# Performance work log

Hardware: AMD Instinct MI355X
Metric: run time of the kernel (lower is better)

The kernel has to match this reference:

```python
import jax, jax.numpy as jnp
import numpy as np

BS = 131072
NX = 4       # num_dim_x (p, theta, v, omega)
NU = 1       # num_dim_control
H = 256      # n_hidden


def segway_dynamics(x):
    # x: [bs, 4] -> f: [bs, 4], g: [bs, 4, 1]
    theta, v, omega = x[:, 1], x[:, 2], x[:, 3]
    c, s = jnp.cos(theta), jnp.sin(theta)
    f2 = (c * (9.8 * s + 11.5 * v) + 68.4 * v - 1.2 * omega ** 2 * s) / (c - 24.7)
    f3 = (-58.8 * v * c - 243.5 * v - s * (208.3 + omega ** 2 * c)) / (c ** 2 - 24.7)
    f = jnp.stack([v, omega, f2, f3], axis=1)
    g2 = (-1.8 * c - 10.9) / (c - 24.7)
    g3 = (9.3 * c + 38.6) / (c ** 2 - 24.7)
    zero = jnp.zeros_like(g2)
    g = jnp.stack([zero, zero, g2, g3], axis=1)[:, :, None]
    return f, g


def setup_inputs() -> dict:
    key = jax.random.key(0)
    ks = jax.random.split(key, 13)
    d = {"x": jax.random.normal(ks[0], (BS, NX), dtype=jnp.float32)}
    shapes = {
        "Vw1": (H, NX), "Vb1": (H,),
        "Vw2": (H, H),  "Vb2": (H,),
        "Vw3": (H // 4, H), "Vb3": (H // 4,),
        "Uw1": (H, NX), "Ub1": (H,),
        "Uw2": (H, H),  "Ub2": (H,),
        "Uw3": (NU, H), "Ub3": (NU,),
    }
    for i, (name, shp) in enumerate(shapes.items()):
        d[name] = jax.random.normal(ks[i + 1], shp, dtype=jnp.float32) * 0.05
    return d


def reference(x, Vw1, Vb1, Vw2, Vb2, Vw3, Vb3, Uw1, Ub1, Uw2, Ub2, Uw3, Ub3):
    # --- Lyapunov value + analytic gradient ---
    a1 = jnp.tanh(x @ Vw1.T + Vb1)          # [bs, H]
    a2 = jnp.tanh(a1 @ Vw2.T + Vb2)         # [bs, H]
    a3 = jnp.tanh(a2 @ Vw3.T + Vb3)         # [bs, H//4]
    V = 0.5 * jnp.sum(a3 * a3, axis=1)      # [bs]
    # diag_embed(1-tanh^2) @ W  ==  (1-tanh^2)[:, :, None] * W  (no dense diag)
    D1 = (1.0 - a1 ** 2)[:, :, None] * Vw1[None]                          # [bs, H, 4]
    D2 = (1.0 - a2 ** 2)[:, :, None] * jnp.einsum('ij,bjk->bik', Vw2, D1)  # [bs, H, 4]
    D3 = (1.0 - a3 ** 2)[:, :, None] * jnp.einsum('ij,bjk->bik', Vw3, D2)  # [bs, H/4, 4]
    grad_V = jnp.einsum('bi,bij->bj', a3, D3)  # [bs, 4]

    # --- learned controls ---
    u1 = jnp.tanh(x @ Uw1.T + Ub1)
    u2 = jnp.tanh(u1 @ Uw2.T + Ub2)
    u = jnp.tanh(u2 @ Uw3.T + Ub3) * 20.0     # [bs, 1]

    # --- Lie derivatives / Vdot ---
    f, g = segway_dynamics(x)
    L_f_V = jnp.sum(grad_V * f, axis=1, keepdims=True)    # [bs, 1]
    L_g_V = jnp.einsum('bi,bic->bc', grad_V, g)           # [bs, 1]
    Vdot = (L_f_V + jnp.sum(L_g_V * u, axis=1, keepdims=True))[:, :, None]  # [bs,1,1]
    return u, V, Vdot
```

## Files before the change

### kernel.cpp

```cpp
#include <hip/hip_runtime.h>
#include <hip/hip_bf16.h>

#define BSZ 131072

typedef __bf16 v8bf __attribute__((ext_vector_type(8)));
typedef float f32x4 __attribute__((ext_vector_type(4)));

constexpr int RPB = 64;
constexpr int NTHREADS = 512;
constexpr int LDA = 264;

constexpr int OFF_B2T = 0;
constexpr int OFF_U2T = 65536;
constexpr int OFF_B2  = 131072;
constexpr int OFF_B3T = 196608;
constexpr int OFF_B3  = 212992;
constexpr int OFF_U3  = 229376;
constexpr int OFF_GV  = 233472;
constexpr int OFF_LV1 = 237568;
constexpr int OFF_LU1 = 245760;
constexpr int WS_ELEMS = 253952;

__device__ __forceinline__ float tanhf_fast(float x){
  float e = __expf(2.0f * x);
  return 1.0f - 2.0f / (e + 1.0f);
}

__device__ __forceinline__ __bf16 f2bf(float f){
  unsigned u = __builtin_bit_cast(unsigned, f);
  u += 0x8000u;
  unsigned short h = (unsigned short)(u >> 16);
  return __builtin_bit_cast(__bf16, h);
}

__global__ void prep_weights(const float* __restrict__ Vw2,
                             const float* __restrict__ Uw2,
                             const float* __restrict__ Vw3,
                             const float* __restrict__ Vw1,
                             const float* __restrict__ Uw1,
                             const float* __restrict__ Uw3,
                             __bf16* __restrict__ ws){
  int e = blockIdx.x * 256 + threadIdx.x;
  if (e >= WS_ELEMS) return;
  int idx, NT, base, mode; const float* W;
  if      (e <  65536){ idx = e;          W = Vw2; mode = 0; NT = 16; base = OFF_B2T; }
  else if (e < 131072){ idx = e - 65536;  W = Uw2; mode = 0; NT = 16; base = OFF_U2T; }
  else if (e < 196608){ idx = e - 131072; W = Vw2; mode = 1; NT = 16; base = OFF_B2;  }
  else if (e < 212992){ idx = e - 196608; W = Vw3; mode = 0; NT = 4;  base = OFF_B3T; }
  else if (e < 229376){ idx = e - 212992; W = Vw3; mode = 1; NT = 16; base = OFF_B3;  }
  else if (e < 233472){ idx = e - 229376; W = Uw3; mode = 2; NT = 1;  base = OFF_U3;  }
  else if (e < 237568){ idx = e - 233472; W = Vw1; mode = 3; NT = 1;  base = OFF_GV;  }
  else if (e < 245760){ idx = e - 237568; W = Vw1; mode = 4; NT = 16; base = OFF_LV1; }
  else                { idx = e - 245760; W = Uw1; mode = 4; NT = 16; base = OFF_LU1; }
  int j = idx & 7, l = (idx >> 3) & 63, f = idx >> 9;
  int nt = f % NT, ks = f / NT;
  int k = ks * 32 + (l >> 4) * 8 + j;
  int n = nt * 16 + (l & 15);
  float v;
  if      (mode == 0) v = W[n * 256 + k];
  else if (mode == 1) v = W[k * 256 + n];
  else if (mode == 2) v = (n == 0) ? W[k] : 0.0f;
  else if (mode == 3) v = (n < 4)  ? W[k * 4 + n] : 0.0f;
  else                v = (k < 4)  ? W[n * 4 + k] : 0.0f;
  ws[base + idx] = f2bf(v);
}

__global__ __launch_bounds__(NTHREADS, 4) void fused_clf(
    const float* __restrict__ x,
    const float* __restrict__ Vb1, const float* __restrict__ Vb2,
    const float* __restrict__ Vb3,
    const float* __restrict__ Ub1, const float* __restrict__ Ub2,
    const float* __restrict__ Ub3,
    const __bf16* __restrict__ ws,
    float* __restrict__ out)
{
  __shared__ __bf16 b1[RPB][LDA];
  __shared__ __bf16 b2[RPB][LDA];
  __shared__ union alignas(16) S3 {
    __bf16 b3[RPB][72];
    float  r4[8][RPB][4];
  } s3;
  __shared__ float  red[RPB][4];
  __shared__ float  utile[RPB];

  const int tid  = threadIdx.x;
  const int lane = tid & 63;
  const int wave = tid >> 6;
  const int quad = lane >> 4;
  const int l16  = lane & 15;
  const int row0 = blockIdx.x * RPB;

  v8bf xa[4];
  #pragma unroll
  for (int m = 0; m < 4; m++){
    v8bf z;
    #pragma unroll
    for (int j = 0; j < 8; j++) z[j] = (__bf16)0.0f;
    if (quad == 0){
      float4 xv = ((const float4*)x)[row0 + m*16 + l16];
      z[0] = f2bf(xv.x); z[1] = f2bf(xv.y); z[2] = f2bf(xv.z); z[3] = f2bf(xv.w);
    }
    xa[m] = z;
  }

  auto layer1m = [&](const __bf16* __restrict__ Bw, const float* __restrict__ bv,
                     __bf16 (*dst)[LDA]){
    const v8bf* B = (const v8bf*)Bw;
    v8bf bf0 = B[(wave*2 + 0)*64 + lane];
    v8bf bf1 = B[(wave*2 + 1)*64 + lane];
    f32x4 acc[4][2];
    #pragma unroll
    for (int m = 0; m < 4; m++){ f32x4 z={0.f,0.f,0.f,0.f}; acc[m][0]=z; acc[m][1]=z; }
    #pragma unroll
    for (int m = 0; m < 4; m++){
      acc[m][0] = __builtin_amdgcn_mfma_f32_16x16x32_bf16(xa[m], bf0, acc[m][0], 0,0,0);
      acc[m][1] = __builtin_amdgcn_mfma_f32_16x16x32_bf16(xa[m], bf1, acc[m][1], 0,0,0);
    }
    #pragma unroll
    for (int m = 0; m < 4; m++){
      int rb = m*16 + quad*4;
      #pragma unroll
      for (int nt = 0; nt < 2; nt++){
        int col = (wave*2 + nt)*16 + l16;
        float bvv = bv[col];
        #pragma unroll
        for (int r = 0; r < 4; r++)
          dst[rb + r][col] = f2bf(tanhf_fast(acc[m][nt][r] + bvv));
      }
    }
  };

  auto gemm256 = [&](const __bf16 (*A)[LDA], const __bf16* __restrict__ Bw,
                     const float* __restrict__ bias, __bf16 (*dst)[LDA], int epi){
    f32x4 acc[4][2];
    #pragma unroll
    for (int m = 0; m < 4; m++){ f32x4 z={0.f,0.f,0.f,0.f}; acc[m][0]=z; acc[m][1]=z; }
    const v8bf* B = (const v8bf*)Bw;
    #pragma unroll
    for (int kk = 0; kk < 8; kk++){
      v8bf a[4];
      #pragma unroll
      for (int m = 0; m < 4; m++)
        a[m] = *(const v8bf*)&A[m*16 + l16][kk*32 + quad*8];
      #pragma unroll
      for (int nt = 0; nt < 2; nt++){
        v8bf bf = B[(kk*16 + wave*2 + nt)*64 + lane];
        #pragma unroll
        for (int m = 0; m < 4; m++)
          acc[m][nt] = __builtin_amdgcn_mfma_f32_16x16x32_bf16(a[m], bf, acc[m][nt], 0,0,0);
      }
    }
    #pragma unroll
    for (int m = 0; m < 4; m++){
      int rb = m*16 + quad*4;
      #pragma unroll
      for (int nt = 0; nt < 2; nt++){
        int col = (wave*2 + nt)*16 + l16;
        float bvv = (epi == 0) ? bias[col] : 0.0f;
        #pragma unroll
        for (int r = 0; r < 4; r++){
          float v = acc[m][nt][r] + bvv;
          if (epi == 0){
            dst[rb + r][col] = f2bf(tanhf_fast(v));
          } else {
            float a1v = (float)dst[rb + r][col];
            dst[rb + r][col] = f2bf(v * (1.0f - a1v*a1v));
          }
        }
      }
    }
  };

  auto mfma_reduce = [&](const __bf16 (*A)[LDA], const __bf16* __restrict__ Bw,
                         int ncols){
    f32x4 acc[4];
    #pragma unroll
    for (int m = 0; m < 4; m++){ f32x4 z={0.f,0.f,0.f,0.f}; acc[m]=z; }
    const v8bf* B = (const v8bf*)Bw;
    v8bf bf = B[wave*64 + lane];
    #pragma unroll
    for (int m = 0; m < 4; m++){
      v8bf a = *(const v8bf*)&A[m*16 + l16][wave*32 + quad*8];
      acc[m] = __builtin_amdgcn_mfma_f32_16x16x32_bf16(a, bf, acc[m], 0,0,0);
    }
    if (l16 < ncols){
      #pragma unroll
      for (int m = 0; m < 4; m++)
        #pragma unroll
        for (int r = 0; r < 4; r++)
          s3.r4[wave][m*16 + quad*4 + r][l16] = acc[m][r];
    }
  };

  layer1m(ws + OFF_LU1, Ub1, b2);
  __syncthreads();
  gemm256(b2, ws + OFF_U2T, Ub2, b1, 0);
  __syncthreads();
  mfma_reduce(b1, ws + OFF_U3, 1);
  __syncthreads();
  if (tid < RPB){
    float z = Ub3[0];
    #pragma unroll
    for (int w = 0; w < 8; w++) z += s3.r4[w][tid][0];
    float u = tanhf_fast(z) * 20.0f;
    utile[tid] = u;
    out[row0 + tid] = u;
  }
  layer1m(ws + OFF_LV1, Vb1, b1);
  __syncthreads();
  gemm256(b1, ws + OFF_B2T, Vb2, b2, 0);
  __syncthreads();

  {
    const int mp = wave >> 2;
    const int nt = wave & 3;
    f32x4 acc[2];
    { f32x4 z={0.f,0.f,0.f,0.f}; acc[0]=z; acc[1]=z; }
    const v8bf* B = (const v8bf*)(ws + OFF_B3T);
    #pragma unroll
    for (int kk = 0; kk < 8; kk++){
      v8bf bf = B[(kk*4 + nt)*64 + lane];
      #pragma unroll
      for (int m2 = 0; m2 < 2; m2++){
        v8bf a = *(const v8bf*)&b2[(mp*2 + m2)*16 + l16][kk*32 + quad*8];
        acc[m2] = __builtin_amdgcn_mfma_f32_16x16x32_bf16(a, bf, acc[m2], 0,0,0);
      }
    }
    int col = nt*16 + l16;
    float bvv = Vb3[col];
    #pragma unroll
    for (int m2 = 0; m2 < 2; m2++){
      #pragma unroll
      for (int r = 0; r < 4; r++){
        int row = (mp*2 + m2)*16 + quad*4 + r;
        float t = tanhf_fast(acc[m2][r] + bvv);
        float sq = t * t;
        sq += __shfl_xor(sq, 1); sq += __shfl_xor(sq, 2);
        sq += __shfl_xor(sq, 4); sq += __shfl_xor(sq, 8);
        s3.b3[row][col] = f2bf(t * (1.0f - t*t));
        if (l16 == 0) red[row][nt] = sq;
      }
    }
  }
  __syncthreads();

  {
    f32x4 acc[4][2];
    #pragma unroll
    for (int m = 0; m < 4; m++){ f32x4 z={0.f,0.f,0.f,0.f}; acc[m][0]=z; acc[m][1]=z; }
    const v8bf* B = (const v8bf*)(ws + OFF_B3);
    #pragma unroll
    for (int kk = 0; kk < 2; kk++){
      v8bf a[4];
      #pragma unroll
      for (int m = 0; m < 4; m++)
        a[m] = *(const v8bf*)&s3.b3[m*16 + l16][kk*32 + quad*8];
      #pragma unroll
      for (int nt = 0; nt < 2; nt++){
        v8bf bf = B[(kk*16 + wave*2 + nt)*64 + lane];
        #pragma unroll
        for (int m = 0; m < 4; m++)
          acc[m][nt] = __builtin_amdgcn_mfma_f32_16x16x32_bf16(a[m], bf, acc[m][nt], 0,0,0);
      }
    }
    #pragma unroll
    for (int m = 0; m < 4; m++){
      int rb = m*16 + quad*4;
      #pragma unroll
      for (int nt = 0; nt < 2; nt++){
        int col = (wave*2 + nt)*16 + l16;
        #pragma unroll
        for (int r = 0; r < 4; r++){
          float a2v = (float)b2[rb + r][col];
          b2[rb + r][col] = f2bf(acc[m][nt][r] * (1.0f - a2v*a2v));
        }
      }
    }
    if (tid < RPB)
      out[BSZ + row0 + tid] = 0.5f * (red[tid][0] + red[tid][1] + red[tid][2] + red[tid][3]);
  }
  __syncthreads();

  gemm256(b2, ws + OFF_B2, nullptr, b1, 1);
  __syncthreads();
  mfma_reduce(b1, ws + OFF_GV, 4);
  __syncthreads();
  if (tid < 256){
    int b = tid >> 2, k2 = tid & 3;
    float s = 0.f;
    #pragma unroll
    for (int w = 0; w < 8; w++) s += s3.r4[w][b][k2];
    red[b][k2] = s;
  }
  __syncthreads();

  if (tid < RPB){
    float4 xv = ((const float4*)x)[row0 + tid];
    float th = xv.y, vv = xv.z, om = xv.w;
    float c = cosf(th), s = sinf(th);
    float dc  = c - 24.7f;
    float dc2 = c*c - 24.7f;
    float f2v = (c*(9.8f*s + 11.5f*vv) + 68.4f*vv - 1.2f*om*om*s) / dc;
    float f3v = (-58.8f*vv*c - 243.5f*vv - s*(208.3f + om*om*c)) / dc2;
    float g2v = (-1.8f*c - 10.9f) / dc;
    float g3v = (9.3f*c + 38.6f) / dc2;
    float Lf = red[tid][0]*vv + red[tid][1]*om + red[tid][2]*f2v + red[tid][3]*f3v;
    float Lg = red[tid][2]*g2v + red[tid][3]*g3v;
    out[2*BSZ + row0 + tid] = Lf + Lg * utile[tid];
  }
}

extern "C" void kernel_launch(void* const* d_in, const int* in_sizes, int n_in,
                              void* d_out, int out_size, void* d_ws, size_t ws_size,
                              hipStream_t stream) {
  const float* x   = (const float*)d_in[0];
  const float* Vw1 = (const float*)d_in[1];
  const float* Vb1 = (const float*)d_in[2];
  const float* Vw2 = (const float*)d_in[3];
  const float* Vb2 = (const float*)d_in[4];
  const float* Vw3 = (const float*)d_in[5];
  const float* Vb3 = (const float*)d_in[6];
  const float* Uw1 = (const float*)d_in[7];
  const float* Ub1 = (const float*)d_in[8];
  const float* Uw2 = (const float*)d_in[9];
  const float* Ub2 = (const float*)d_in[10];
  const float* Uw3 = (const float*)d_in[11];
  const float* Ub3 = (const float*)d_in[12];
  __bf16* ws = (__bf16*)d_ws;
  float* out = (float*)d_out;

  hipLaunchKernelGGL(prep_weights, dim3((WS_ELEMS + 255) / 256), dim3(256), 0, stream,
                     Vw2, Uw2, Vw3, Vw1, Uw1, Uw3, ws);
  hipLaunchKernelGGL(fused_clf, dim3(BSZ / RPB), dim3(NTHREADS), 0, stream,
                     x, Vb1, Vb2, Vb3, Ub1, Ub2, Ub3, ws, out);
}
```

Baseline: 198.4 us.

## Swap MFMA operand roles to weights-as-A, halve rows per block, pack bf16 stores

Reorients every MFMA so weights are the A operand and batch activations the B operand, which makes accumulator registers run along the feature dimension. Epilogues can then write four contiguous bf16 values with one packed store instead of scattered scalar stores. Rows per block drop from 64 to 32 and the occupancy hint rises to 8 blocks per CU, trading weight reuse per block for more resident blocks. The weight-prep kernel now writes eight elements per thread with vector stores.

```diff
diff --git a/kernel.cpp b/kernel.cpp
--- a/kernel.cpp
+++ b/kernel.cpp
@@ -4,21 +4,23 @@
 #define BSZ 131072
 
 typedef __bf16 v8bf __attribute__((ext_vector_type(8)));
+typedef __bf16 v4bf __attribute__((ext_vector_type(4)));
 typedef float f32x4 __attribute__((ext_vector_type(4)));
 
-constexpr int RPB = 64;
+constexpr int RPB = 32;
 constexpr int NTHREADS = 512;
-constexpr int LDA = 264;
-
-constexpr int OFF_B2T = 0;
-constexpr int OFF_U2T = 65536;
-constexpr int OFF_B2  = 131072;
-constexpr int OFF_B3T = 196608;
-constexpr int OFF_B3  = 212992;
+constexpr int LDA  = 264;
+constexpr int LDA3 = 72;
+
+constexpr int OFF_U2  = 0;
+constexpr int OFF_V2  = 65536;
+constexpr int OFF_V2T = 131072;
+constexpr int OFF_V3  = 196608;
+constexpr int OFF_V3T = 212992;
 constexpr int OFF_U3  = 229376;
 constexpr int OFF_GV  = 233472;
-constexpr int OFF_LV1 = 237568;
-constexpr int OFF_LU1 = 245760;
+constexpr int OFF_L1V = 237568;
+constexpr int OFF_L1U = 245760;
 constexpr int WS_ELEMS = 253952;
 
 __device__ __forceinline__ float tanhf_fast(float x){
@@ -31,6 +33,12 @@
   u += 0x8000u;
   unsigned short h = (unsigned short)(u >> 16);
   return __builtin_bit_cast(__bf16, h);
+}
+
+__device__ __forceinline__ unsigned pack2bf(float lo, float hi){
+  unsigned a = __builtin_bit_cast(unsigned, lo) + 0x8000u;
+  unsigned b = __builtin_bit_cast(unsigned, hi) + 0x8000u;
+  return __builtin_amdgcn_perm(b, a, 0x07060302u);
 }
 
 __global__ void prep_weights(const float* __restrict__ Vw2,
@@ -40,32 +48,39 @@
                              const float* __restrict__ Uw1,
                              const float* __restrict__ Uw3,
                              __bf16* __restrict__ ws){
-  int e = blockIdx.x * 256 + threadIdx.x;
-  if (e >= WS_ELEMS) return;
-  int idx, NT, base, mode; const float* W;
-  if      (e <  65536){ idx = e;          W = Vw2; mode = 0; NT = 16; base = OFF_B2T; }
-  else if (e < 131072){ idx = e - 65536;  W = Uw2; mode = 0; NT = 16; base = OFF_U2T; }
-  else if (e < 196608){ idx = e - 131072; W = Vw2; mode = 1; NT = 16; base = OFF_B2;  }
-  else if (e < 212992){ idx = e - 196608; W = Vw3; mode = 0; NT = 4;  base = OFF_B3T; }
-  else if (e < 229376){ idx = e - 212992; W = Vw3; mode = 1; NT = 16; base = OFF_B3;  }
-  else if (e < 233472){ idx = e - 229376; W = Uw3; mode = 2; NT = 1;  base = OFF_U3;  }
-  else if (e < 237568){ idx = e - 233472; W = Vw1; mode = 3; NT = 1;  base = OFF_GV;  }
-  else if (e < 245760){ idx = e - 237568; W = Vw1; mode = 4; NT = 16; base = OFF_LV1; }
-  else                { idx = e - 245760; W = Uw1; mode = 4; NT = 16; base = OFF_LU1; }
-  int j = idx & 7, l = (idx >> 3) & 63, f = idx >> 9;
-  int nt = f % NT, ks = f / NT;
-  int k = ks * 32 + (l >> 4) * 8 + j;
-  int n = nt * 16 + (l & 15);
-  float v;
-  if      (mode == 0) v = W[n * 256 + k];
-  else if (mode == 1) v = W[k * 256 + n];
-  else if (mode == 2) v = (n == 0) ? W[k] : 0.0f;
-  else if (mode == 3) v = (n < 4)  ? W[k * 4 + n] : 0.0f;
-  else                v = (k < 4)  ? W[n * 4 + k] : 0.0f;
-  ws[base + idx] = f2bf(v);
-}
-
-__global__ __launch_bounds__(NTHREADS, 4) void fused_clf(
+  int e8 = blockIdx.x * 256 + threadIdx.x;
+  if (e8 >= WS_ELEMS / 8) return;
+  int idx8 = e8 * 8;
+  int idx, MT, mode; const float* W;
+  if      (idx8 <  65536){ idx = idx8;          W = Uw2; mode = 0; MT = 16; }
+  else if (idx8 < 131072){ idx = idx8 - 65536;  W = Vw2; mode = 0; MT = 16; }
+  else if (idx8 < 196608){ idx = idx8 - 131072; W = Vw2; mode = 1; MT = 16; }
+  else if (idx8 < 212992){ idx = idx8 - 196608; W = Vw3; mode = 0; MT = 4;  }
+  else if (idx8 < 229376){ idx = idx8 - 212992; W = Vw3; mode = 1; MT = 16; }
+  else if (idx8 < 233472){ idx = idx8 - 229376; W = Uw3; mode = 2; MT = 1;  }
+  else if (idx8 < 237568){ idx = idx8 - 233472; W = Vw1; mode = 3; MT = 1;  }
+  else if (idx8 < 245760){ idx = idx8 - 237568; W = Vw1; mode = 4; MT = 16; }
+  else                   { idx = idx8 - 245760; W = Uw1; mode = 4; MT = 16; }
+  int l = (idx >> 3) & 63, f = idx >> 9;
+  int mt = f % MT, ks = f / MT;
+  int m  = mt * 16 + (l & 15);
+  int k0 = ks * 32 + ((l >> 4) << 3);
+  __bf16 tmp[8];
+  #pragma unroll
+  for (int j = 0; j < 8; j++){
+    int k = k0 + j;
+    float v;
+    if      (mode == 0) v = W[m * 256 + k];
+    else if (mode == 1) v = W[k * 256 + m];
+    else if (mode == 2) v = (m == 0) ? W[k] : 0.0f;
+    else if (mode == 3) v = (m < 4)  ? W[k * 4 + m] : 0.0f;
+    else                v = (k < 4)  ? W[m * 4 + k] : 0.0f;
+    tmp[j] = f2bf(v);
+  }
+  *(uint4*)&ws[idx8] = *(const uint4*)tmp;
+}
+
+__global__ __launch_bounds__(NTHREADS, 8) void fused_clf(
     const float* __restrict__ x,
     const float* __restrict__ Vb1, const float* __restrict__ Vb2,
     const float* __restrict__ Vb3,
@@ -74,14 +89,14 @@
     const __bf16* __restrict__ ws,
     float* __restrict__ out)
 {
-  __shared__ __bf16 b1[RPB][LDA];
-  __shared__ __bf16 b2[RPB][LDA];
+  __shared__ alignas(16) __bf16 b1[RPB][LDA];
+  __shared__ alignas(16) __bf16 b2[RPB][LDA];
   __shared__ union alignas(16) S3 {
-    __bf16 b3[RPB][72];
+    __bf16 b3[RPB][LDA3];
     float  r4[8][RPB][4];
   } s3;
-  __shared__ float  red[RPB][4];
-  __shared__ float  utile[RPB];
+  __shared__ float red[RPB][4];
+  __shared__ float utile[RPB];
 
   const int tid  = threadIdx.x;
   const int lane = tid & 63;
@@ -90,113 +105,117 @@
   const int l16  = lane & 15;
   const int row0 = blockIdx.x * RPB;
 
-  v8bf xa[4];
+  v8bf xb[2];
   #pragma unroll
-  for (int m = 0; m < 4; m++){
+  for (int bt = 0; bt < 2; bt++){
     v8bf z;
     #pragma unroll
     for (int j = 0; j < 8; j++) z[j] = (__bf16)0.0f;
     if (quad == 0){
-      float4 xv = ((const float4*)x)[row0 + m*16 + l16];
+      float4 xv = ((const float4*)x)[row0 + bt*16 + l16];
       z[0] = f2bf(xv.x); z[1] = f2bf(xv.y); z[2] = f2bf(xv.z); z[3] = f2bf(xv.w);
     }
-    xa[m] = z;
-  }
-
-  auto layer1m = [&](const __bf16* __restrict__ Bw, const float* __restrict__ bv,
+    xb[bt] = z;
+  }
+
+  auto layer1m = [&](const __bf16* __restrict__ Aw, const float* __restrict__ bv,
                      __bf16 (*dst)[LDA]){
-    const v8bf* B = (const v8bf*)Bw;
-    v8bf bf0 = B[(wave*2 + 0)*64 + lane];
-    v8bf bf1 = B[(wave*2 + 1)*64 + lane];
-    f32x4 acc[4][2];
-    #pragma unroll
-    for (int m = 0; m < 4; m++){ f32x4 z={0.f,0.f,0.f,0.f}; acc[m][0]=z; acc[m][1]=z; }
-    #pragma unroll
-    for (int m = 0; m < 4; m++){
-      acc[m][0] = __builtin_amdgcn_mfma_f32_16x16x32_bf16(xa[m], bf0, acc[m][0], 0,0,0);
-      acc[m][1] = __builtin_amdgcn_mfma_f32_16x16x32_bf16(xa[m], bf1, acc[m][1], 0,0,0);
-    }
-    #pragma unroll
-    for (int m = 0; m < 4; m++){
-      int rb = m*16 + quad*4;
-      #pragma unroll
-      for (int nt = 0; nt < 2; nt++){
-        int col = (wave*2 + nt)*16 + l16;
-        float bvv = bv[col];
+    const v8bf* A = (const v8bf*)Aw;
+    #pragma unroll
+    for (int mi = 0; mi < 2; mi++){
+      v8bf af = A[(wave*2 + mi)*64 + lane];
+      f32x4 acc[2];
+      { f32x4 z = {0.f,0.f,0.f,0.f}; acc[0]=z; acc[1]=z; }
+      #pragma unroll
+      for (int bt = 0; bt < 2; bt++)
+        acc[bt] = __builtin_amdgcn_mfma_f32_16x16x32_bf16(af, xb[bt], acc[bt], 0,0,0);
+      int f0 = (wave*2 + mi)*16 + quad*4;
+      float4 bv4 = *(const float4*)&bv[f0];
+      #pragma unroll
+      for (int bt = 0; bt < 2; bt++){
+        int b = bt*16 + l16;
+        float t0 = tanhf_fast(acc[bt][0] + bv4.x);
+        float t1 = tanhf_fast(acc[bt][1] + bv4.y);
+        float t2 = tanhf_fast(acc[bt][2] + bv4.z);
+        float t3 = tanhf_fast(acc[bt][3] + bv4.w);
+        uint2 p = { pack2bf(t0, t1), pack2bf(t2, t3) };
+        *(uint2*)&dst[b][f0] = p;
+      }
+    }
+  };
+
+  auto gemmW = [&](const __bf16* __restrict__ Aw, const __bf16 (*act)[LDA],
+                   const float* __restrict__ bias, __bf16 (*dst)[LDA], int epi){
+    f32x4 acc[2][2];
+    #pragma unroll
+    for (int mi = 0; mi < 2; mi++){ f32x4 z={0.f,0.f,0.f,0.f}; acc[mi][0]=z; acc[mi][1]=z; }
+    const v8bf* A = (const v8bf*)Aw;
+    #pragma unroll
+    for (int kk = 0; kk < 8; kk++){
+      v8bf bf[2];
+      #pragma unroll
+      for (int bt = 0; bt < 2; bt++)
+        bf[bt] = *(const v8bf*)&act[bt*16 + l16][kk*32 + quad*8];
+      #pragma unroll
+      for (int mi = 0; mi < 2; mi++){
+        v8bf af = A[(kk*16 + wave*2 + mi)*64 + lane];
         #pragma unroll
-        for (int r = 0; r < 4; r++)
-          dst[rb + r][col] = f2bf(tanhf_fast(acc[m][nt][r] + bvv));
+        for (int bt = 0; bt < 2; bt++)
+          acc[mi][bt] = __builtin_amdgcn_mfma_f32_16x16x32_bf16(af, bf[bt], acc[mi][bt], 0,0,0);
+      }
+    }
+    #pragma unroll
+    for (int mi = 0; mi < 2; mi++){
+      int f0 = (wave*2 + mi)*16 + quad*4;
+      float4 bv4 = (epi == 0) ? *(const float4*)&bias[f0] : float4{0,0,0,0};
+      #pragma unroll
+      for (int bt = 0; bt < 2; bt++){
+        int b = bt*16 + l16;
+        if (epi == 0){
+          float t0 = tanhf_fast(acc[mi][bt][0] + bv4.x);
+          float t1 = tanhf_fast(acc[mi][bt][1] + bv4.y);
+          float t2 = tanhf_fast(acc[mi][bt][2] + bv4.z);
+          float t3 = tanhf_fast(acc[mi][bt][3] + bv4.w);
+          uint2 p = { pack2bf(t0, t1), pack2bf(t2, t3) };
+          *(uint2*)&dst[b][f0] = p;
+        } else {
+          v4bf a4 = *(const v4bf*)&dst[b][f0];
+          float v0 = acc[mi][bt][0] * (1.0f - (float)a4[0]*(float)a4[0]);
+          float v1 = acc[mi][bt][1] * (1.0f - (float)a4[1]*(float)a4[1]);
+          float v2 = acc[mi][bt][2] * (1.0f - (float)a4[2]*(float)a4[2]);
+          float v3 = acc[mi][bt][3] * (1.0f - (float)a4[3]*(float)a4[3]);
+          uint2 p = { pack2bf(v0, v1), pack2bf(v2, v3) };
+          *(uint2*)&dst[b][f0] = p;
+        }
       }
     }
   };
 
-  auto gemm256 = [&](const __bf16 (*A)[LDA], const __bf16* __restrict__ Bw,
-                     const float* __restrict__ bias, __bf16 (*dst)[LDA], int epi){
-    f32x4 acc[4][2];
-    #pragma unroll
-    for (int m = 0; m < 4; m++){ f32x4 z={0.f,0.f,0.f,0.f}; acc[m][0]=z; acc[m][1]=z; }
-    const v8bf* B = (const v8bf*)Bw;
-    #pragma unroll
-    for (int kk = 0; kk < 8; kk++){
-      v8bf a[4];
-      #pragma unroll
-      for (int m = 0; m < 4; m++)
-        a[m] = *(const v8bf*)&A[m*16 + l16][kk*32 + quad*8];
-      #pragma unroll
-      for (int nt = 0; nt < 2; nt++){
-        v8bf bf = B[(kk*16 + wave*2 + nt)*64 + lane];
-        #pragma unroll
-        for (int m = 0; m < 4; m++)
-          acc[m][nt] = __builtin_amdgcn_mfma_f32_16x16x32_bf16(a[m], bf, acc[m][nt], 0,0,0);
-      }
-    }
-    #pragma unroll
-    for (int m = 0; m < 4; m++){
-      int rb = m*16 + quad*4;
-      #pragma unroll
-      for (int nt = 0; nt < 2; nt++){
-        int col = (wave*2 + nt)*16 + l16;
-        float bvv = (epi == 0) ? bias[col] : 0.0f;
-        #pragma unroll
-        for (int r = 0; r < 4; r++){
-          float v = acc[m][nt][r] + bvv;
-          if (epi == 0){
-            dst[rb + r][col] = f2bf(tanhf_fast(v));
-          } else {
-            float a1v = (float)dst[rb + r][col];
-            dst[rb + r][col] = f2bf(v * (1.0f - a1v*a1v));
-          }
-        }
+  auto mfma_reduce = [&](const __bf16 (*act)[LDA], const __bf16* __restrict__ Aw,
+                         bool four){
+    const v8bf* A = (const v8bf*)Aw;
+    v8bf af = A[wave*64 + lane];
+    f32x4 acc[2];
+    { f32x4 z = {0.f,0.f,0.f,0.f}; acc[0]=z; acc[1]=z; }
+    #pragma unroll
+    for (int bt = 0; bt < 2; bt++){
+      v8bf bf = *(const v8bf*)&act[bt*16 + l16][wave*32 + quad*8];
+      acc[bt] = __builtin_amdgcn_mfma_f32_16x16x32_bf16(af, bf, acc[bt], 0,0,0);
+    }
+    if (quad == 0){
+      #pragma unroll
+      for (int bt = 0; bt < 2; bt++){
+        if (four) *(f32x4*)&s3.r4[wave][bt*16 + l16][0] = acc[bt];
+        else      s3.r4[wave][bt*16 + l16][0] = acc[bt][0];
       }
     }
   };
 
-  auto mfma_reduce = [&](const __bf16 (*A)[LDA], const __bf16* __restrict__ Bw,
-                         int ncols){
-    f32x4 acc[4];
-    #pragma unroll
-    for (int m = 0; m < 4; m++){ f32x4 z={0.f,0.f,0.f,0.f}; acc[m]=z; }
-    const v8bf* B = (const v8bf*)Bw;
-    v8bf bf = B[wave*64 + lane];
-    #pragma unroll
-    for (int m = 0; m < 4; m++){
-      v8bf a = *(const v8bf*)&A[m*16 + l16][wave*32 + quad*8];
-      acc[m] = __builtin_amdgcn_mfma_f32_16x16x32_bf16(a, bf, acc[m], 0,0,0);
-    }
-    if (l16 < ncols){
-      #pragma unroll
-      for (int m = 0; m < 4; m++)
-        #pragma unroll
-        for (int r = 0; r < 4; r++)
-          s3.r4[wave][m*16 + quad*4 + r][l16] = acc[m][r];
-    }
-  };
-
-  layer1m(ws + OFF_LU1, Ub1, b2);
-  __syncthreads();
-  gemm256(b2, ws + OFF_U2T, Ub2, b1, 0);
-  __syncthreads();
-  mfma_reduce(b1, ws + OFF_U3, 1);
+  layer1m(ws + OFF_L1U, Ub1, b2);
+  __syncthreads();
+  gemmW(ws + OFF_U2, b2, Ub2, b1, 0);
+  __syncthreads();
+  mfma_reduce(b1, ws + OFF_U3, false);
   __syncthreads();
   if (tid < RPB){
     float z = Ub3[0];
@@ -206,74 +225,70 @@
     utile[tid] = u;
     out[row0 + tid] = u;
   }
-  layer1m(ws + OFF_LV1, Vb1, b1);
-  __syncthreads();
-  gemm256(b1, ws + OFF_B2T, Vb2, b2, 0);
+  layer1m(ws + OFF_L1V, Vb1, b1);
+  __syncthreads();
+  gemmW(ws + OFF_V2, b1, Vb2, b2, 0);
   __syncthreads();
 
   {
-    const int mp = wave >> 2;
-    const int nt = wave & 3;
-    f32x4 acc[2];
-    { f32x4 z={0.f,0.f,0.f,0.f}; acc[0]=z; acc[1]=z; }
-    const v8bf* B = (const v8bf*)(ws + OFF_B3T);
+    const int mt = wave & 3, bt = wave >> 2;
+    f32x4 acc = {0.f,0.f,0.f,0.f};
+    const v8bf* A = (const v8bf*)(ws + OFF_V3);
     #pragma unroll
     for (int kk = 0; kk < 8; kk++){
-      v8bf bf = B[(kk*4 + nt)*64 + lane];
-      #pragma unroll
-      for (int m2 = 0; m2 < 2; m2++){
-        v8bf a = *(const v8bf*)&b2[(mp*2 + m2)*16 + l16][kk*32 + quad*8];
-        acc[m2] = __builtin_amdgcn_mfma_f32_16x16x32_bf16(a, bf, acc[m2], 0,0,0);
-      }
-    }
-    int col = nt*16 + l16;
-    float bvv = Vb3[col];
-    #pragma unroll
-    for (int m2 = 0; m2 < 2; m2++){
-      #pragma unroll
-      for (int r = 0; r < 4; r++){
-        int row = (mp*2 + m2)*16 + quad*4 + r;
-        float t = tanhf_fast(acc[m2][r] + bvv);
-        float sq = t * t;
-        sq += __shfl_xor(sq, 1); sq += __shfl_xor(sq, 2);
-        sq += __shfl_xor(sq, 4); sq += __shfl_xor(sq, 8);
-        s3.b3[row][col] = f2bf(t * (1.0f - t*t));
-        if (l16 == 0) red[row][nt] = sq;
-      }
-    }
+      v8bf bf = *(const v8bf*)&b2[bt*16 + l16][kk*32 + quad*8];
+      v8bf af = A[(kk*4 + mt)*64 + lane];
+      acc = __builtin_amdgcn_mfma_f32_16x16x32_bf16(af, bf, acc, 0,0,0);
+    }
+    int f0 = mt*16 + quad*4;
+    int b  = bt*16 + l16;
+    float4 bv4 = *(const float4*)&Vb3[f0];
+    float t0 = tanhf_fast(acc[0] + bv4.x);
+    float t1 = tanhf_fast(acc[1] + bv4.y);
+    float t2 = tanhf_fast(acc[2] + bv4.z);
+    float t3 = tanhf_fast(acc[3] + bv4.w);
+    float sq = t0*t0 + t1*t1 + t2*t2 + t3*t3;
+    uint2 p = { pack2bf(t0*(1.0f-t0*t0), t1*(1.0f-t1*t1)),
+                pack2bf(t2*(1.0f-t2*t2), t3*(1.0f-t3*t3)) };
+    *(uint2*)&s3.b3[b][f0] = p;
+    sq += __shfl_xor(sq, 16);
+    sq += __shfl_xor(sq, 32);
+    if (lane < 16) red[b][mt] = sq;
   }
   __syncthreads();
 
   {
-    f32x4 acc[4][2];
-    #pragma unroll
-    for (int m = 0; m < 4; m++){ f32x4 z={0.f,0.f,0.f,0.f}; acc[m][0]=z; acc[m][1]=z; }
-    const v8bf* B = (const v8bf*)(ws + OFF_B3);
+    f32x4 acc[2][2];
+    #pragma unroll
+    for (int mi = 0; mi < 2; mi++){ f32x4 z={0.f,0.f,0.f,0.f}; acc[mi][0]=z; acc[mi][1]=z; }
+    const v8bf* A = (const v8bf*)(ws + OFF_V3T);
     #pragma unroll
     for (int kk = 0; kk < 2; kk++){
-      v8bf a[4];
-      #pragma unroll
-      for (int m = 0; m < 4; m++)
-        a[m] = *(const v8bf*)&s3.b3[m*16 + l16][kk*32 + quad*8];
-      #pragma unroll
-      for (int nt = 0; nt < 2; nt++){
-        v8bf bf = B[(kk*16 + wave*2 + nt)*64 + lane];
+      v8bf bf[2];
+      #pragma unroll
+      for (int bt = 0; bt < 2; bt++)
+        bf[bt] = *(const v8bf*)&s3.b3[bt*16 + l16][kk*32 + quad*8];
+      #pragma unroll
+      for (int mi = 0; mi < 2; mi++){
+        v8bf af = A[(kk*16 + wave*2 + mi)*64 + lane];
         #pragma unroll
-        for (int m = 0; m < 4; m++)
-          acc[m][nt] = __builtin_amdgcn_mfma_f32_16x16x32_bf16(a[m], bf, acc[m][nt], 0,0,0);
-      }
-    }
-    #pragma unroll
-    for (int m = 0; m < 4; m++){
-      int rb = m*16 + quad*4;
-      #pragma unroll
-      for (int nt = 0; nt < 2; nt++){
-        int col = (wave*2 + nt)*16 + l16;
-        #pragma unroll
-        for (int r = 0; r < 4; r++){
-          float a2v = (float)b2[rb + r][col];
-          b2[rb + r][col] = f2bf(acc[m][nt][r] * (1.0f - a2v*a2v));
-        }
+        for (int bt = 0; bt < 2; bt++)
+          acc[mi][bt] = __builtin_amdgcn_mfma_f32_16x16x32_bf16(af, bf[bt], acc[mi][bt], 0,0,0);
+      }
+    }
+    #pragma unroll
+    for (int mi = 0; mi < 2; mi++){
+      int f0 = (wave*2 + mi)*16 + quad*4;
+      #pragma unroll
+      for (int bt = 0; bt < 2; bt++){
+        int b = bt*16 + l16;
+        v4bf a4 = *(const v4bf*)&b2[b][f0];
+        float v0 = acc[mi][bt][0] * (1.0f - (float)a4[0]*(float)a4[0]);
+        float v1 = acc[mi][bt][1] * (1.0f - (float)a4[1]*(float)a4[1]);
+        float v2 = acc[mi][bt][2] * (1.0f - (float)a4[2]*(float)a4[2]);
+        float v3 = acc[mi][bt][3] * (1.0f - (float)a4[3]*(float)a4[3]);
+        uint2 p = { pack2bf(v0, v1), pack2bf(v2, v3) };
+        *(uint2*)&b2[b][f0] = p;
       }
     }
     if (tid < RPB)
@@ -281,16 +296,16 @@
   }
   __syncthreads();
 
-  gemm256(b2, ws + OFF_B2, nullptr, b1, 1);
-  __syncthreads();
-  mfma_reduce(b1, ws + OFF_GV, 4);
-  __syncthreads();
-  if (tid < 256){
-    int b = tid >> 2, k2 = tid & 3;
+  gemmW(ws + OFF_V2T, b2, nullptr, b1, 1);
+  __syncthreads();
+  mfma_reduce(b1, ws + OFF_GV, true);
+  __syncthreads();
+  if (tid < 4*RPB){
+    int b = tid >> 2, j = tid & 3;
     float s = 0.f;
     #pragma unroll
-    for (int w = 0; w < 8; w++) s += s3.r4[w][b][k2];
-    red[b][k2] = s;
+    for (int w = 0; w < 8; w++) s += s3.r4[w][b][j];
+    red[b][j] = s;
   }
   __syncthreads();
 
@@ -329,7 +344,7 @@
   __bf16* ws = (__bf16*)d_ws;
   float* out = (float*)d_out;
 
-  hipLaunchKernelGGL(prep_weights, dim3((WS_ELEMS + 255) / 256), dim3(256), 0, stream,
+  hipLaunchKernelGGL(prep_weights, dim3((WS_ELEMS/8 + 255) / 256), dim3(256), 0, stream,
                      Vw2, Uw2, Vw3, Vw1, Uw1, Uw3, ws);
   hipLaunchKernelGGL(fused_clf, dim3(BSZ / RPB), dim3(NTHREADS), 0, stream,
                      x, Vb1, Vb2, Vb3, Ub1, Ub2, Ub3, ws, out);
```

Result: slower. 212.1 us (+6.9%).
